# Optimization experiments

Hardware: AMD Instinct MI355X
Metric: run time of the kernel (lower is better)

Reference implementation:

```python
import jax, jax.numpy as jnp
import numpy as np

ALPHA = 0.1  # GCN2 initial-residual strength (PyG default)


def _gcn2_layer(x, row, col, w, W, n_nodes):
    # symmetric normalization with self-loops already appended to (row, col, w)
    deg = jax.ops.segment_sum(w, col, num_segments=n_nodes)
    dinv = jnp.where(deg > 0, jax.lax.rsqrt(deg), 0.0)
    norm = dinv[row] * w * dinv[col]                      # [E+N]
    msg = x[col] * norm[:, None]                          # gather: [E+N, C]
    agg = jax.ops.segment_sum(msg, row, num_segments=n_nodes)  # scatter: [N, C]
    h = (1.0 - ALPHA) * agg + ALPHA * x                   # initial residual (x0 = x)
    return h @ W


def setup_inputs() -> dict:
    key = jax.random.key(0)
    k1, k2, k3, k4 = jax.random.split(key, 4)
    N, E, C = 100000, 1200000, 64
    x = jax.random.normal(k1, (N, C), dtype=jnp.float32)
    edge_index = jax.random.randint(k2, (2, E), 0, N, dtype=jnp.int64)
    edge_weight = jax.random.uniform(k3, (E,), dtype=jnp.float32)
    W1 = jax.random.normal(k4, (C, C), dtype=jnp.float32) / np.sqrt(C)
    return {"x": x, "edge_index": edge_index, "edge_weight": edge_weight, "W1": W1}


def reference(x, edge_index, edge_weight, W1):
    N = x.shape[0]
    loops = jnp.arange(N, dtype=edge_index.dtype)
    row = jnp.concatenate([edge_index[0], loops])
    col = jnp.concatenate([edge_index[1], loops])
    w = jnp.concatenate([edge_weight, jnp.ones((N,), dtype=x.dtype)])
    # dropout is identity in eval mode (training=False)
    out = _gcn2_layer(x, row, col, w, W1, N)
    return jax.nn.relu(out)
```

## Files before the change

kernel.cpp:

```cpp
#include <hip/hip_runtime.h>

constexpr int C = 64;
constexpr int C4 = 16;
constexpr int NBLK   = 256;
constexpr int MAXBUK = 512;
constexpr int DCAP   = 4352;
constexpr float WFX_SCALE   = 16777216.0f;
constexpr float WFX_INV     = 1.0f / 16777216.0f;

__device__ __forceinline__ unsigned short f2bf(float f) {
    unsigned b = __float_as_uint(f);
    return (unsigned short)((b + 0x7FFFu + ((b >> 16) & 1u)) >> 16);
}
__device__ __forceinline__ float bf2f(unsigned u) {
    return __uint_as_float(u << 16);
}

__global__ __launch_bounds__(256) void k_hist(const int* __restrict__ row,
                                              const int* __restrict__ col, int E,
                                              int nbuk,
                                              int* __restrict__ slotR,
                                              int* __restrict__ slotC) {
    __shared__ int hR[MAXBUK], hC[MAXBUK];
    for (int i = threadIdx.x; i < nbuk; i += 256) { hR[i] = 0; hC[i] = 0; }
    __syncthreads();
    const int epb = (E + NBLK - 1) / NBLK;
    const int beg = blockIdx.x * epb;
    const int end = min(beg + epb, E);
    for (int i = beg + threadIdx.x; i < end; i += 256) {
        atomicAdd(&hR[row[i] >> 8], 1);
        atomicAdd(&hC[col[i] >> 8], 1);
    }
    __syncthreads();
    for (int b = threadIdx.x; b < nbuk; b += 256) {
        slotR[blockIdx.x * nbuk + b] = hR[b];
        slotC[blockIdx.x * nbuk + b] = hC[b];
    }
}

__global__ __launch_bounds__(256) void k_scanBlk(int* __restrict__ slotR,
                                                 int* __restrict__ slotC,
                                                 int nbuk,
                                                 int* __restrict__ gCntR,
                                                 int* __restrict__ gCntC) {
    __shared__ int s[NBLK];
    const int t = threadIdx.x;
    const int b = blockIdx.x;
    int v = slotR[t * nbuk + b];
    s[t] = v;
    __syncthreads();
    for (int d = 1; d < NBLK; d <<= 1) {
        int o = (t >= d) ? s[t - d] : 0; __syncthreads();
        s[t] += o; __syncthreads();
    }
    slotR[t * nbuk + b] = s[t] - v;
    if (t == NBLK - 1) gCntR[b] = s[NBLK - 1];
    __syncthreads();
    v = slotC[t * nbuk + b];
    s[t] = v;
    __syncthreads();
    for (int d = 1; d < NBLK; d <<= 1) {
        int o = (t >= d) ? s[t - d] : 0; __syncthreads();
        s[t] += o; __syncthreads();
    }
    slotC[t * nbuk + b] = s[t] - v;
    if (t == NBLK - 1) gCntC[b] = s[NBLK - 1];
}

__global__ __launch_bounds__(512) void k_scan2(const int* __restrict__ gCntR,
                                               const int* __restrict__ gCntC,
                                               int* __restrict__ gBaseR,
                                               int* __restrict__ gBaseC, int nbuk,
                                               int* __restrict__ rowptrN) {
    __shared__ int s[512];
    int t = threadIdx.x;
    int v = (t < nbuk) ? gCntR[t] : 0;
    s[t] = v;
    __syncthreads();
    for (int d = 1; d < 512; d <<= 1) {
        int o = (t >= d) ? s[t - d] : 0; __syncthreads();
        s[t] += o; __syncthreads();
    }
    if (t < nbuk) gBaseR[t] = s[t] - v;
    if (t == nbuk - 1) { gBaseR[nbuk] = s[t]; rowptrN[0] = s[t]; }
    __syncthreads();
    int v2 = (t < nbuk) ? gCntC[t] : 0;
    s[t] = v2;
    __syncthreads();
    for (int d = 1; d < 512; d <<= 1) {
        int o = (t >= d) ? s[t - d] : 0; __syncthreads();
        s[t] += o; __syncthreads();
    }
    if (t < nbuk) gBaseC[t] = s[t] - v2;
    if (t == nbuk - 1) gBaseC[nbuk] = s[t];
}

__global__ __launch_bounds__(256) void k_place(const int* __restrict__ row,
                                               const int* __restrict__ col,
                                               const float* __restrict__ w, int E,
                                               int nbuk,
                                               const int* __restrict__ gBaseR,
                                               const int* __restrict__ gBaseC,
                                               const int* __restrict__ slotR,
                                               const int* __restrict__ slotC,
                                               int2* __restrict__ tmpR,
                                               int* __restrict__ tmpC) {
    __shared__ int cR[MAXBUK], cC[MAXBUK];
    __shared__ int bR[MAXBUK], bC[MAXBUK];
    for (int i = threadIdx.x; i < nbuk; i += 256) {
        cR[i] = 0; cC[i] = 0;
        bR[i] = gBaseR[i] + slotR[blockIdx.x * nbuk + i];
        bC[i] = gBaseC[i] + slotC[blockIdx.x * nbuk + i];
    }
    __syncthreads();
    const int epb = (E + NBLK - 1) / NBLK;
    const int beg = blockIdx.x * epb;
    const int end = min(beg + epb, E);
    for (int i = beg + threadIdx.x; i < end; i += 256) {
        int r = row[i], c = col[i];
        float ww = w[i];
        int kR = r >> 8, kC = c >> 8;
        int pR = bR[kR] + atomicAdd(&cR[kR], 1);
        int pC = bC[kC] + atomicAdd(&cC[kC], 1);
        int wfx = (int)fminf(ww * WFX_SCALE, WFX_SCALE - 1.0f);
        tmpR[pR] = make_int2(((r & 255) << 24) | c, __float_as_int(ww));
        tmpC[pC] = ((c & 255) << 24) | wfx;
    }
}

__global__ __launch_bounds__(256) void k_build(const int* __restrict__ tmpC,
                                               const int* __restrict__ gBaseC,
                                               int2* __restrict__ tmpR,
                                               const int* __restrict__ gBaseR,
                                               const float4* __restrict__ x4, int N,
                                               float* __restrict__ dinv,
                                               ushort* __restrict__ xbs,
                                               int* __restrict__ rowptr) {
    __shared__ int degI[256];
    __shared__ float dloc[256];
    __shared__ int cntRow[256], scanBuf[256], exclA[256], curA[256];
    __shared__ int   lcol[DCAP];
    __shared__ float lcoef[DCAP];
    const int b = blockIdx.x, t = threadIdx.x;
    const int r0 = b << 8;

    degI[t] = 0;
    __syncthreads();
    const int cbase = gBaseC[b];
    const int ccnt  = gBaseC[b + 1] - cbase;
    for (int i = t; i < ccnt; i += 256) {
        int rec = tmpC[cbase + i];
        atomicAdd(&degI[(unsigned)rec >> 24], rec & 0xFFFFFF);
    }
    __syncthreads();
    float deg = (float)degI[t] * WFX_INV;
    float dv = rsqrtf(deg + 1.0f);
    dloc[t] = dv;
    if (r0 + t < N) dinv[r0 + t] = dv;
    __syncthreads();
    #pragma unroll
    for (int it = 0; it < 16; ++it) {
        int f  = t + it * 256;
        int vl = f >> 4, c4 = f & 15;
        int vv = r0 + vl;
        if (vv < N) {
            float s = dloc[vl];
            float4 xv = x4[(size_t)vv * C4 + c4];
            ushort4 o;
            o.x = f2bf(xv.x * s); o.y = f2bf(xv.y * s);
            o.z = f2bf(xv.z * s); o.w = f2bf(xv.w * s);
            *(ushort4*)(xbs + (size_t)vv * C + c4 * 4) = o;
        }
    }

    cntRow[t] = 0;
    __syncthreads();
    const int base = gBaseR[b];
    const int cnt  = gBaseR[b + 1] - base;
    for (int i = t; i < cnt; i += 256)
        atomicAdd(&cntRow[((unsigned)tmpR[base + i].x) >> 24], 1);
    __syncthreads();
    int v = cntRow[t];
    scanBuf[t] = v;
    __syncthreads();
    for (int d = 1; d < 256; d <<= 1) {
        int o = (t >= d) ? scanBuf[t - d] : 0; __syncthreads();
        scanBuf[t] += o; __syncthreads();
    }
    exclA[t] = scanBuf[t] - v;
    curA[t]  = exclA[t];
    __syncthreads();
    for (int i = t; i < cnt; i += 256) {
        int2 rec = tmpR[base + i];
        unsigned rx = (unsigned)rec.x;
        int r8 = rx >> 24;
        int p = atomicAdd(&curA[r8], 1);
        if (p < DCAP) {
            lcol[p]  = (int)(rx & 0xFFFFFF);
            lcoef[p] = dloc[r8] * __int_as_float(rec.y);
        }
    }
    __syncthreads();
    for (int i = t; i < cnt; i += 256)
        tmpR[base + i] = make_int2(lcol[i], __float_as_int(lcoef[i]));
    if (r0 + t < N) rowptr[r0 + t] = base + exclA[t];
}

__global__ __launch_bounds__(256) void k_gather(const int* __restrict__ rowptr,
                                                const int2* __restrict__ epack,
                                                const ushort* __restrict__ xbs,
                                                const float* __restrict__ dinv,
                                                float* __restrict__ h, int N) {
    int v = (blockIdx.x * blockDim.x + threadIdx.x) >> 6;
    int lane = threadIdx.x & 63;
    if (v >= N) return;
    int beg = __builtin_amdgcn_readfirstlane(rowptr[v]);
    int end = __builtin_amdgcn_readfirstlane(rowptr[v + 1]);
    float dv  = dinv[v];
    float rdv = 1.0f / dv;
    float xbv = bf2f(xbs[(size_t)v * C + lane]);
    float acc = dv * xbv;
    int j = beg;
    for (; j + 7 < end; j += 8) {
        int2 m0 = epack[j],     m1 = epack[j + 1];
        int2 m2 = epack[j + 2], m3 = epack[j + 3];
        int2 m4 = epack[j + 4], m5 = epack[j + 5];
        int2 m6 = epack[j + 6], m7 = epack[j + 7];
        float x0 = bf2f(xbs[(size_t)m0.x * C + lane]);
        float x1 = bf2f(xbs[(size_t)m1.x * C + lane]);
        float x2 = bf2f(xbs[(size_t)m2.x * C + lane]);
        float x3 = bf2f(xbs[(size_t)m3.x * C + lane]);
        float x4v = bf2f(xbs[(size_t)m4.x * C + lane]);
        float x5 = bf2f(xbs[(size_t)m5.x * C + lane]);
        float x6 = bf2f(xbs[(size_t)m6.x * C + lane]);
        float x7 = bf2f(xbs[(size_t)m7.x * C + lane]);
        acc += __int_as_float(m0.y) * x0;
        acc += __int_as_float(m1.y) * x1;
        acc += __int_as_float(m2.y) * x2;
        acc += __int_as_float(m3.y) * x3;
        acc += __int_as_float(m4.y) * x4v;
        acc += __int_as_float(m5.y) * x5;
        acc += __int_as_float(m6.y) * x6;
        acc += __int_as_float(m7.y) * x7;
    }
    for (; j + 3 < end; j += 4) {
        int2 m0 = epack[j],     m1 = epack[j + 1];
        int2 m2 = epack[j + 2], m3 = epack[j + 3];
        float x0 = bf2f(xbs[(size_t)m0.x * C + lane]);
        float x1 = bf2f(xbs[(size_t)m1.x * C + lane]);
        float x2 = bf2f(xbs[(size_t)m2.x * C + lane]);
        float x3 = bf2f(xbs[(size_t)m3.x * C + lane]);
        acc += __int_as_float(m0.y) * x0;
        acc += __int_as_float(m1.y) * x1;
        acc += __int_as_float(m2.y) * x2;
        acc += __int_as_float(m3.y) * x3;
    }
    for (; j < end; ++j) {
        int2 m = epack[j];
        acc += __int_as_float(m.y) * bf2f(xbs[(size_t)m.x * C + lane]);
    }
    h[(size_t)v * C + lane] = 0.9f * acc + 0.1f * xbv * rdv;
}

__global__ __launch_bounds__(256, 4) void k_mm(float4* __restrict__ io4,
                                               const float4* __restrict__ W4, int N) {
    __shared__ float Ws[C * C];
    __shared__ float hs[64 * 68];
    const int tid = threadIdx.x;
    const int base = blockIdx.x * 64;

    #pragma unroll
    for (int i = 0; i < 4; ++i) {
        int f = tid + i * 256;
        ((float4*)Ws)[f] = W4[f];
    }
    #pragma unroll
    for (int i = 0; i < 4; ++i) {
        int f = tid + i * 256;
        int vl = f >> 4, c4 = f & 15;
        int v = base + vl;
        float4 hv;
        if (v < N) hv = io4[(size_t)v * C4 + c4];
        else       hv.x = hv.y = hv.z = hv.w = 0.0f;
        *(float4*)&hs[vl * 68 + c4 * 4] = hv;
    }
    __syncthreads();

    const int tc = tid & 15;
    const int tn = tid >> 4;
    float4 acc[4];
    #pragma unroll
    for (int i = 0; i < 4; ++i) { acc[i].x = acc[i].y = acc[i].z = acc[i].w = 0.0f; }

    #pragma unroll 2
    for (int k4 = 0; k4 < 16; ++k4) {
        float4 wv0 = *(const float4*)&Ws[(k4 * 4 + 0) * C + tc * 4];
        float4 wv1 = *(const float4*)&Ws[(k4 * 4 + 1) * C + tc * 4];
        float4 wv2 = *(const float4*)&Ws[(k4 * 4 + 2) * C + tc * 4];
        float4 wv3 = *(const float4*)&Ws[(k4 * 4 + 3) * C + tc * 4];
        #pragma unroll
        for (int i = 0; i < 4; ++i) {
            float4 hv = *(const float4*)&hs[(tn * 4 + i) * 68 + k4 * 4];
            acc[i].x += hv.x * wv0.x + hv.y * wv1.x + hv.z * wv2.x + hv.w * wv3.x;
            acc[i].y += hv.x * wv0.y + hv.y * wv1.y + hv.z * wv2.y + hv.w * wv3.y;
            acc[i].z += hv.x * wv0.z + hv.y * wv1.z + hv.z * wv2.z + hv.w * wv3.z;
            acc[i].w += hv.x * wv0.w + hv.y * wv1.w + hv.z * wv2.w + hv.w * wv3.w;
        }
    }

    #pragma unroll
    for (int i = 0; i < 4; ++i) {
        int v = base + tn * 4 + i;
        if (v < N) {
            float4 o;
            o.x = fmaxf(acc[i].x, 0.0f);
            o.y = fmaxf(acc[i].y, 0.0f);
            o.z = fmaxf(acc[i].z, 0.0f);
            o.w = fmaxf(acc[i].w, 0.0f);
            io4[(size_t)v * C4 + tc] = o;
        }
    }
}

extern "C" void kernel_launch(void* const* d_in, const int* in_sizes, int n_in,
                              void* d_out, int out_size, void* d_ws, size_t ws_size,
                              hipStream_t stream) {
    const float* x  = (const float*)d_in[0];
    const int*   ei = (const int*)d_in[1];
    const float* ew_in = (const float*)d_in[2];
    const float* W  = (const float*)d_in[3];

    const int N = in_sizes[0] / C;
    const int E = in_sizes[1] / 2;
    const int* row = ei;
    const int* col = ei + E;
    float* out = (float*)d_out;

    const int nbuk = (N + 255) >> 8;

    int*    wsI    = (int*)d_ws;
    int2*   tmpR   = (int2*)wsI;
    int*    tmpC   = wsI + (size_t)E * 2;
    ushort* xbs    = (ushort*)(wsI + (size_t)E * 3);
    int*    regC   = wsI + (size_t)E * 3 + (size_t)N * C / 2;
    int*    rowptr = regC;
    float*  dinv   = (float*)(rowptr + (N + 1));
    int*    gCntR  = (int*)(dinv + N);
    int*    gCntC  = gCntR + MAXBUK;
    int*    gBaseR = gCntC + MAXBUK;
    int*    gBaseC = gBaseR + (MAXBUK + 1);
    int*    slotR  = gBaseC + (MAXBUK + 1);
    int*    slotC  = slotR + NBLK * MAXBUK;

    k_hist  <<<NBLK, 256, 0, stream>>>(row, col, E, nbuk, slotR, slotC);
    k_scanBlk<<<nbuk, NBLK, 0, stream>>>(slotR, slotC, nbuk, gCntR, gCntC);
    k_scan2 <<<1, 512, 0, stream>>>(gCntR, gCntC, gBaseR, gBaseC, nbuk, rowptr + N);
    k_place <<<NBLK, 256, 0, stream>>>(row, col, ew_in, E, nbuk, gBaseR, gBaseC,
                                       slotR, slotC, tmpR, tmpC);
    k_build <<<nbuk, 256, 0, stream>>>(tmpC, gBaseC, tmpR, gBaseR,
                                       (const float4*)x, N, dinv, xbs, rowptr);
    k_gather<<<(N * 64 + 255) / 256, 256, 0, stream>>>(rowptr, (const int2*)tmpR,
                                                       xbs, dinv, out, N);
    k_mm    <<<(N + 63) / 64, 256, 0, stream>>>((float4*)out, (const float4*)W, N);
}
```

Baseline: 123.0 us.

## Stage bucket scatter through shared memory for contiguous global writes in k_place

```diff
diff --git a/kernel.cpp b/kernel.cpp
--- a/kernel.cpp
+++ b/kernel.cpp
@@ -4,6 +4,7 @@
 constexpr int C4 = 16;
 constexpr int NBLK   = 256;
 constexpr int MAXBUK = 512;
+constexpr int MAXEPB = 5120;
 constexpr int DCAP   = 4352;
 constexpr float WFX_SCALE   = 16777216.0f;
 constexpr float WFX_INV     = 1.0f / 16777216.0f;
@@ -105,26 +106,93 @@
                                                const int* __restrict__ slotC,
                                                int2* __restrict__ tmpR,
                                                int* __restrict__ tmpC) {
-    __shared__ int cR[MAXBUK], cC[MAXBUK];
-    __shared__ int bR[MAXBUK], bC[MAXBUK];
-    for (int i = threadIdx.x; i < nbuk; i += 256) {
-        cR[i] = 0; cC[i] = 0;
-        bR[i] = gBaseR[i] + slotR[blockIdx.x * nbuk + i];
-        bC[i] = gBaseC[i] + slotC[blockIdx.x * nbuk + i];
-    }
-    __syncthreads();
+    __shared__ int2 bufR[MAXEPB];
+    __shared__ unsigned short bIdx[MAXEPB];
+    __shared__ int hcnt[MAXBUK], excl[MAXBUK], cur[MAXBUK];
+    __shared__ int addC[MAXBUK], runB[MAXBUK];
+    __shared__ int pairS[256];
+    const int t   = threadIdx.x;
+    const int blk = blockIdx.x;
     const int epb = (E + NBLK - 1) / NBLK;
-    const int beg = blockIdx.x * epb;
+    const int beg = blk * epb;
     const int end = min(beg + epb, E);
-    for (int i = beg + threadIdx.x; i < end; i += 256) {
-        int r = row[i], c = col[i];
-        float ww = w[i];
-        int kR = r >> 8, kC = c >> 8;
-        int pR = bR[kR] + atomicAdd(&cR[kR], 1);
-        int pC = bC[kC] + atomicAdd(&cC[kC], 1);
-        int wfx = (int)fminf(ww * WFX_SCALE, WFX_SCALE - 1.0f);
-        tmpR[pR] = make_int2(((r & 255) << 24) | c, __float_as_int(ww));
-        tmpC[pC] = ((c & 255) << 24) | wfx;
+
+    for (int i = t; i < nbuk; i += 256) runB[i] = gBaseR[i] + slotR[blk * nbuk + i];
+    __syncthreads();
+    for (int s = beg; s < end; s += MAXEPB) {
+        const int n = min(MAXEPB, end - s);
+        for (int i = t; i < MAXBUK; i += 256) hcnt[i] = 0;
+        __syncthreads();
+        for (int i = t; i < n; i += 256) atomicAdd(&hcnt[row[s + i] >> 8], 1);
+        __syncthreads();
+        int pa = hcnt[2 * t], pb = hcnt[2 * t + 1];
+        int pv = pa + pb;
+        pairS[t] = pv;
+        __syncthreads();
+        for (int d = 1; d < 256; d <<= 1) {
+            int o = (t >= d) ? pairS[t - d] : 0; __syncthreads();
+            pairS[t] += o; __syncthreads();
+        }
+        int ep = pairS[t] - pv;
+        excl[2 * t] = ep;      excl[2 * t + 1] = ep + pa;
+        cur[2 * t]  = ep;      cur[2 * t + 1]  = ep + pa;
+        __syncthreads();
+        for (int i = t; i < MAXBUK; i += 256) addC[i] = runB[i] - excl[i];
+        __syncthreads();
+        for (int i = t; i < n; i += 256) {
+            int r = row[s + i], c = col[s + i];
+            float ww = w[s + i];
+            int b = r >> 8;
+            int p = atomicAdd(&cur[b], 1);
+            bufR[p] = make_int2(((r & 255) << 24) | c, __float_as_int(ww));
+            bIdx[p] = (unsigned short)b;
+        }
+        __syncthreads();
+        for (int i = t; i < n; i += 256)
+            tmpR[addC[bIdx[i]] + i] = bufR[i];
+        __syncthreads();
+        for (int i = t; i < MAXBUK; i += 256) runB[i] += hcnt[i];
+        __syncthreads();
+    }
+
+    int* bufC = (int*)bufR;
+    for (int i = t; i < nbuk; i += 256) runB[i] = gBaseC[i] + slotC[blk * nbuk + i];
+    __syncthreads();
+    for (int s = beg; s < end; s += MAXEPB) {
+        const int n = min(MAXEPB, end - s);
+        for (int i = t; i < MAXBUK; i += 256) hcnt[i] = 0;
+        __syncthreads();
+        for (int i = t; i < n; i += 256) atomicAdd(&hcnt[col[s + i] >> 8], 1);
+        __syncthreads();
+        int pa = hcnt[2 * t], pb = hcnt[2 * t + 1];
+        int pv = pa + pb;
+        pairS[t] = pv;
+        __syncthreads();
+        for (int d = 1; d < 256; d <<= 1) {
+            int o = (t >= d) ? pairS[t - d] : 0; __syncthreads();
+            pairS[t] += o; __syncthreads();
+        }
+        int ep = pairS[t] - pv;
+        excl[2 * t] = ep;      excl[2 * t + 1] = ep + pa;
+        cur[2 * t]  = ep;      cur[2 * t + 1]  = ep + pa;
+        __syncthreads();
+        for (int i = t; i < MAXBUK; i += 256) addC[i] = runB[i] - excl[i];
+        __syncthreads();
+        for (int i = t; i < n; i += 256) {
+            int c = col[s + i];
+            float ww = w[s + i];
+            int b = c >> 8;
+            int p = atomicAdd(&cur[b], 1);
+            int wfx = (int)fminf(ww * WFX_SCALE, WFX_SCALE - 1.0f);
+            bufC[p] = ((c & 255) << 24) | wfx;
+            bIdx[p] = (unsigned short)b;
+        }
+        __syncthreads();
+        for (int i = t; i < n; i += 256)
+            tmpC[addC[bIdx[i]] + i] = bufC[i];
+        __syncthreads();
+        for (int i = t; i < MAXBUK; i += 256) runB[i] += hcnt[i];
+        __syncthreads();
     }
 }
 
```

After: 130.3 us. 6.0% more time.
